# Optimization experiments

Measured on AMD Instinct MI355X. Metric: run time of the kernel, lower is better.

## Reference

```python
import jax, jax.numpy as jnp
import numpy as np

NZ = 128
N_GEN = 8
BATCH = 2048
SLOPE = 0.2


def _convt(x, w, b, stride, pad):
    # PyTorch ConvTranspose2d(weight [Cin,Cout,kH,kW], stride, padding p)
    # == conv with lhs_dilation=stride, padding=k-1-p, spatially-flipped
    # kernel with in/out channels swapped.
    k = jnp.flip(w, axis=(2, 3)).transpose(2, 3, 0, 1)  # [kH,kW,Cin,Cout]
    y = jax.lax.conv_general_dilated(
        x, k, window_strides=(1, 1), padding=[(pad, pad), (pad, pad)],
        lhs_dilation=(stride, stride),
        dimension_numbers=('NCHW', 'HWIO', 'NCHW'))
    return y + b[None, :, None, None]


def setup_inputs() -> dict:
    key = jax.random.key(0)
    ks = jax.random.split(key, 12)
    s = 0.05
    return {
        'z': jax.random.normal(ks[0], (BATCH, NZ), jnp.float32),
        'g_idx': jax.random.randint(ks[1], (BATCH,), 0, N_GEN),
        'W1': jax.random.normal(ks[2], (N_GEN, NZ, 256), jnp.float32) * s,
        'b1': jax.random.normal(ks[3], (N_GEN, 256), jnp.float32) * s,
        'W2': jax.random.normal(ks[4], (N_GEN, 256, 1568), jnp.float32) * s,
        'b2': jax.random.normal(ks[5], (N_GEN, 1568), jnp.float32) * s,
        'cw1': jax.random.normal(ks[6], (N_GEN, 32, 16, 4, 4), jnp.float32) * s,
        'cb1': jax.random.normal(ks[7], (N_GEN, 16), jnp.float32) * s,
        'cw2': jax.random.normal(ks[8], (N_GEN, 16, 8, 4, 4), jnp.float32) * s,
        'cb2': jax.random.normal(ks[9], (N_GEN, 8), jnp.float32) * s,
        'cw3': jax.random.normal(ks[10], (N_GEN, 8, 1, 3, 3), jnp.float32) * s,
        'cb3': jax.random.normal(ks[11], (N_GEN, 1), jnp.float32) * s,
    }


def _single_gen(params, z):
    W1, b1, W2, b2, cw1, cb1, cw2, cb2, cw3, cb3 = params
    lrelu = lambda x: jax.nn.leaky_relu(x, SLOPE)
    h = lrelu(z @ W1 + b1)                 # [B,256]
    h = lrelu(h @ W2 + b2)                 # [B,1568]
    h = h.reshape(-1, 32, 7, 7)
    h = lrelu(_convt(h, cw1, cb1, 2, 2))   # [B,16,14,14]
    h = lrelu(_convt(h, cw2, cb2, 2, 2))   # [B,8,28,28]
    return jnp.tanh(_convt(h, cw3, cb3, 1, 1))  # [B,1,28,28]


def reference(z, g_idx, W1, b1, W2, b2, cw1, cb1, cw2, cb2, cw3, cb3):
    params = (W1, b1, W2, b2, cw1, cb1, cw2, cb2, cw3, cb3)
    # Compute every generator on the full batch (faithful to the torch loop),
    # vmapped over the generator axis: images [G,B,1,28,28].
    images = jax.vmap(_single_gen, in_axes=((0,) * 10, None))(params, z)
    # Per-sample gather: keep generator g_idx[b] for each sample b.
    return images[g_idx, jnp.arange(z.shape[0])]
```

## Files before the change

### kernel.cpp

```cpp
#include <hip/hip_runtime.h>
#include <cstdint>
#include <cstddef>

#define BATCH 2048
#define NZ 128
#define NGEN 8
#define GRPS 32
#define MAXG 72
#define NCT 13
#define H2_ELEMS 1792
#define WS_H1_OFF 16384
#define WS_H2_OFF (16384 + MAXG * 8192 * 4)
#define WS_W2T_OFF (WS_H2_OFF + BATCH * H2_ELEMS * 2)
#define W2T_GSTRIDE (1568 * 256)
#define NB_W2T (NGEN * 49)
#define NB_PREP (NB_W2T + MAXG * 4)
#define WS_WPK1_OFF (WS_W2T_OFF + NGEN * W2T_GSTRIDE * 2)
#define WS_WPK2_OFF (WS_WPK1_OFF + NGEN * 4096 * 4)
#define WS_WPK3_OFF (WS_WPK2_OFF + NGEN * 1024 * 4)

typedef unsigned int u32;
typedef unsigned short u16;
typedef unsigned long long u64;
typedef _Float16 f16x8 __attribute__((ext_vector_type(8)));
typedef _Float16 f16x4 __attribute__((ext_vector_type(4)));
typedef _Float16 f16x2 __attribute__((ext_vector_type(2)));
typedef float f32x4 __attribute__((ext_vector_type(4)));

__device__ __forceinline__ float lrelu(float x) { return fmaxf(x, 0.2f * x); }
__device__ __forceinline__ u16 f16b(float f) {
    _Float16 h = (_Float16)f;
    return __builtin_bit_cast(u16, h);
}
__device__ __forceinline__ u32 pk2(float a, float b) {
    f16x2 v; v[0] = (_Float16)a; v[1] = (_Float16)b;
    return __builtin_bit_cast(u32, v);
}
__device__ __forceinline__ float dot2(u32 a, u32 b, float c) {
#if __has_builtin(__builtin_amdgcn_fdot2)
    return __builtin_amdgcn_fdot2(__builtin_bit_cast(f16x2, a),
                                  __builtin_bit_cast(f16x2, b), c, false);
#else
    float d;
    asm("v_dot2_f32_f16 %0, %1, %2, %3" : "=v"(d) : "v"(a), "v"(b), "v"(c));
    return d;
#endif
}
__device__ __forceinline__ float fast_tanh(float x) {
    x = fminf(fmaxf(x, -9.f), 9.f);
    const float e = __expf(2.f * x);
    return (e - 1.f) / (e + 1.f);
}

__global__ void bin_kernel(const int* __restrict__ g_idx, int* __restrict__ wsi) {
    __shared__ int wcnt[4][NGEN];
    __shared__ int wboff[4][NGEN];
    __shared__ int pbase[NGEN + 1];
    __shared__ u16 rank[BATCH];
    const int tid = threadIdx.x;
    const int w = tid >> 6, lane = tid & 63;
    if (tid < 4 * NGEN) wcnt[tid >> 3][tid & 7] = 0;
    __syncthreads();
    const u64 lt = ((u64)1 << lane) - 1;
    #pragma unroll
    for (int r = 0; r < 8; ++r) {
        const int b = r * 256 + tid;
        const int gg = g_idx[b];
        u64 m[NGEN];
        #pragma unroll
        for (int k = 0; k < NGEN; ++k) m[k] = __ballot(gg == k);
        rank[b] = (u16)((int)__popcll(m[gg] & lt) + wcnt[w][gg]);
        if (lane < NGEN) wcnt[w][lane] += (int)__popcll(m[lane]);
    }
    __syncthreads();
    if (tid == 0) {
        int acc = 0;
        for (int g = 0; g < NGEN; ++g) {
            pbase[g] = acc;
            const int tot = wcnt[0][g] + wcnt[1][g] + wcnt[2][g] + wcnt[3][g];
            acc += ((tot + GRPS - 1) / GRPS) * GRPS;
        }
        pbase[NGEN] = acc;
        wsi[0] = acc;
    }
    __syncthreads();
    if (tid < 32) {
        const int ww = tid >> 3, g = tid & 7;
        int off = pbase[g];
        for (int w2 = 0; w2 < ww; ++w2) off += wcnt[w2][g];
        wboff[ww][g] = off;
    }
    const int total = pbase[NGEN];
    for (int i = tid; i < total; i += 256) wsi[16 + i] = -1;
    __syncthreads();
    #pragma unroll
    for (int r = 0; r < 8; ++r) {
        const int b = r * 256 + tid;
        const int gg = g_idx[b];
        wsi[16 + wboff[w][gg] + (int)rank[b]] = b;
    }
}

__global__ __launch_bounds__(256) void prep_kernel(
    const float* __restrict__ z, const int* __restrict__ g_idx,
    const float* __restrict__ W1, const float* __restrict__ b1,
    const float* __restrict__ W2, const int* __restrict__ wsi,
    float* __restrict__ h1g, _Float16* __restrict__ W2T,
    const float* __restrict__ cw1, const float* __restrict__ cw2,
    const float* __restrict__ cw3,
    u32* __restrict__ wpk1, u32* __restrict__ wpk2, u32* __restrict__ wpk3)
{
    __shared__ _Float16 t[32][264];
    __shared__ float zst[NZ][12];
    __shared__ int sb[8];
    __shared__ int sG;

    const int tid = threadIdx.x;
    const int bx = blockIdx.x;

    if (bx >= NB_PREP) {
        const int g = bx - NB_PREP;
        const float* c1p = cw1 + g * 8192;
        u32* o1 = wpk1 + g * 4096;
        for (int i = tid; i < 4096; i += 256) {
            const int cip = i >> 8, a = (i >> 6) & 3, co = (i >> 2) & 15, c = i & 3;
            const float* s = c1p + cip * 512 + co * 16 + a * 4 + c;
            o1[i] = pk2(s[0], s[256]);
        }
        const float* c2p = cw2 + g * 2048;
        u32* o2 = wpk2 + g * 1024;
        for (int i = tid; i < 1024; i += 256) {
            const int cip = i >> 7, a = (i >> 5) & 3, co = (i >> 2) & 7, c = i & 3;
            const float* s = c2p + cip * 256 + co * 16 + a * 4 + c;
            o2[i] = pk2(s[0], s[128]);
        }
        if (tid < 36) {
            const int cip = tid / 9, r = tid % 9;
            const float* s = cw3 + g * 72 + cip * 18 + r;
            wpk3[g * 36 + tid] = pk2(s[0], s[9]);
        }
        return;
    }

    if (bx < NB_W2T) {
        const int g = bx / 49;
        const int n0 = (bx % 49) * 32;
        const float* src = W2 + (size_t)g * 256 * 1568;
        const int nl = tid & 31, kh = tid >> 5;
        #pragma unroll 8
        for (int p = 0; p < 32; ++p) {
            const int k = p * 8 + kh;
            t[nl][k] = (_Float16)src[(size_t)k * 1568 + n0 + nl];
        }
        __syncthreads();
        _Float16* dst = W2T + (size_t)g * W2T_GSTRIDE + (size_t)n0 * 256;
        const int n = tid >> 3, k0 = (tid & 7) * 32;
        #pragma unroll
        for (int j = 0; j < 4; ++j)
            *(uint4*)(dst + (size_t)n * 256 + k0 + 8 * j) = *(const uint4*)&t[n][k0 + 8 * j];
        return;
    }

    const int bx2 = bx - NB_W2T;
    const int grp = bx2 >> 2;
    const int s0 = (bx2 & 3) * 8;
    if (grp * GRPS >= wsi[0]) return;

    if (tid == 0) sG = g_idx[wsi[16 + grp * GRPS]];
    if (tid < 8) sb[tid] = wsi[16 + grp * GRPS + s0 + tid];
    __syncthreads();
    const float* W1g = W1 + sG * (NZ * 256);
    const float* b1g = b1 + sG * 256;

    {
        const int s = tid >> 5, f = tid & 31;
        float4 v = make_float4(0.f, 0.f, 0.f, 0.f);
        if (sb[s] >= 0) v = *(const float4*)(z + (size_t)sb[s] * NZ + 4 * f);
        zst[4 * f + 0][s] = v.x; zst[4 * f + 1][s] = v.y;
        zst[4 * f + 2][s] = v.z; zst[4 * f + 3][s] = v.w;
    }
    __syncthreads();

    const int c = tid;
    float acc[8];
    #pragma unroll
    for (int s = 0; s < 8; ++s) acc[s] = 0.f;
    const float* wp = W1g + c;
    #pragma unroll 4
    for (int k = 0; k < NZ; ++k) {
        const float w = wp[k * 256];
        float av[8];
        *(float4*)&av[0] = *(const float4*)&zst[k][0];
        *(float4*)&av[4] = *(const float4*)&zst[k][4];
        #pragma unroll
        for (int s = 0; s < 8; ++s) acc[s] += av[s] * w;
    }
    const float bv = b1g[c];
    float* hp = h1g + (size_t)grp * 8192 + (size_t)s0 * 256 + c;
    #pragma unroll
    for (int s = 0; s < 8; ++s) hp[s * 256] = lrelu(acc[s] + bv);
}

__global__ __launch_bounds__(256) void fc2_kernel(
    const int* __restrict__ g_idx,
    const _Float16* __restrict__ W2T, const float* __restrict__ b2,
    const int* __restrict__ wsi, const float* __restrict__ h1g,
    u16* __restrict__ h2g)
{
    __shared__ _Float16 afrag[2 * 8 * 64 * 8];
    __shared__ int sb[GRPS];
    __shared__ int sG;

    const int tid = threadIdx.x;
    const int grp = blockIdx.x / NCT;
    const int tile = blockIdx.x % NCT;
    if (grp * GRPS >= wsi[0]) return;

    if (tid == 0) sG = g_idx[wsi[16 + grp * GRPS]];
    if (tid < GRPS) sb[tid] = wsi[16 + grp * GRPS + tid];
    __syncthreads();
    const _Float16* W2Tg = W2T + (size_t)sG * W2T_GSTRIDE;
    const float* b2g = b2 + sG * 1568;

    {
        const float4* h1p4 = (const float4*)(h1g + (size_t)grp * 8192);
        #pragma unroll
        for (int i = 0; i < 8; ++i) {
            const int u = tid + 256 * i;
            const int j4 = u & 1;
            const int ln = (u >> 1) & 63;
            const int kq = (u >> 7) & 7;
            const int mt = (u >> 10) & 1;
            const int s = mt * 16 + (ln & 15);
            const float4 v = h1p4[s * 64 + kq * 8 + ((ln >> 4) << 1) + j4];
            f16x4 hi;
            hi[0] = (_Float16)v.x; hi[1] = (_Float16)v.y;
            hi[2] = (_Float16)v.z; hi[3] = (_Float16)v.w;
            const int bh = ((mt * 8 + kq) * 64 + ln) * 8 + 4 * j4;
            *(f16x4*)&afrag[bh] = hi;
        }
    }
    __syncthreads();

    const int wave = tid >> 6;
    const int lane = tid & 63;
    const int q = lane >> 4;
    const int nl = lane & 15;
    const int nb0 = tile * 128 + 2 * wave * 16;
    if (nb0 >= 1568) return;

    #pragma unroll
    for (int nt = 0; nt < 2; ++nt) {
        const int nb = nb0 + nt * 16;
        if (nb >= 1568) break;
        const int n = nb + nl;
        const _Float16* bp = W2Tg + (size_t)n * 256 + q * 8;
        f32x4 accA = {0.f, 0.f, 0.f, 0.f}, accB = accA;
        #pragma unroll
        for (int kq = 0; kq < 8; ++kq) {
            const f16x8 b = *(const f16x8*)(bp + kq * 32);
            const f16x8 a0 = *(const f16x8*)&afrag[((0 * 8 + kq) * 64 + lane) * 8];
            const f16x8 a1 = *(const f16x8*)&afrag[((1 * 8 + kq) * 64 + lane) * 8];
            accA = __builtin_amdgcn_mfma_f32_16x16x32_f16(a0, b, accA, 0, 0, 0);
            accB = __builtin_amdgcn_mfma_f32_16x16x32_f16(a1, b, accB, 0, 0, 0);
        }
        const float bias = b2g[n];
        const int ci = n / 49, rm = n % 49;
        const int off = ci * 56 + (rm / 7) * 8 + (rm % 7);
        #pragma unroll
        for (int mt = 0; mt < 2; ++mt) {
            const f32x4 a = (mt == 0) ? accA : accB;
            #pragma unroll
            for (int reg = 0; reg < 4; ++reg) {
                const int s = mt * 16 + q * 4 + reg;
                const int bb = sb[s];
                if (bb >= 0)
                    h2g[(size_t)bb * H2_ELEMS + off] = f16b(lrelu(a[reg] + bias));
            }
        }
    }
}

template <int H>
__device__ __forceinline__ void conv2p_half(
    const u32 (*c1s)[14][20], u16* dst,
    const u32* __restrict__ w2g, const float bv, const int co, const int y)
{
    float acc[14];
    #pragma unroll
    for (int xx = 0; xx < 14; ++xx) acc[xx] = bv;
    const int a0 = (y + 1) & 1;
    for (int aa = 0; aa < 2; ++aa) {
        const int a = a0 + 2 * aa;
        const int iy = (y + 1 - a) >> 1;
        if ((unsigned)iy < 14u) {
            #pragma unroll 2
            for (int cip = 0; cip < 8; ++cip) {
                u32 rr[10];
                if (H == 0) {
                    *(uint4*)&rr[0] = *(const uint4*)&c1s[cip][iy][0];
                    *(uint4*)&rr[4] = *(const uint4*)&c1s[cip][iy][4];
                } else {
                    *(uint4*)&rr[0] = *(const uint4*)&c1s[cip][iy][4];
                    *(uint4*)&rr[4] = *(const uint4*)&c1s[cip][iy][8];
                    *(uint2*)&rr[8] = *(const uint2*)&c1s[cip][iy][12];
                }
                const uint4 wq = *(const uint4*)(w2g + ((cip * 4 + a) * 8 + co) * 4);
                const u32 wv[4] = {wq.x, wq.y, wq.z, wq.w};
                #pragma unroll
                for (int xx = 0; xx < 14; ++xx) {
                    const int x = 14 * H + xx;
                    const int c0v = (x + 1) & 1;
                    const int ix0 = (x + 1 - c0v) >> 1;
                    const int li = ix0 - 4 * H;
                    if (ix0 < 14) acc[xx] = dot2(rr[li],     wv[c0v],     acc[xx]);
                    if (ix0 >= 1) acc[xx] = dot2(rr[li - 1], wv[c0v + 2], acc[xx]);
                }
            }
        }
    }
    #pragma unroll
    for (int xx = 0; xx < 14; ++xx) dst[2 * (14 * H + xx)] = f16b(lrelu(acc[xx]));
}

__global__ __launch_bounds__(256, 7) void conv_kernel(
    const int* __restrict__ g_idx,
    const u32* __restrict__ wpk1, const float* __restrict__ cb1,
    const u32* __restrict__ wpk2, const float* __restrict__ cb2,
    const u32* __restrict__ wpk3, const float* __restrict__ cb3,
    const u16* __restrict__ h2g, float* __restrict__ out)
{
    __shared__ __align__(16) char smem[8960 + 12992];
    u32 (*c1s)[14][20] = (u32 (*)[14][20])smem;
    u32 (*h2s)[7][8]   = (u32 (*)[7][8])(smem + 8960);
    u32 (*c2s)[28][29] = (u32 (*)[28][29])(smem + 8960);
    __shared__ u32 w3s[36];

    const int tid = threadIdx.x;
    const int b = blockIdx.x;
    const int g = g_idx[b];
    const u32* w1g = wpk1 + g * 4096;
    const u32* w2g = wpk2 + g * 1024;
    const float* cb1g = cb1 + g * 16;
    const float* cb2g = cb2 + g * 8;
    const float  cb3v = cb3[g];

    if (tid < 224) {
        const uint4 qv = ((const uint4*)(h2g + (size_t)b * H2_ELEMS))[tid];
        const int ci = tid / 7, yq = tid % 7;
        u16* dst = (u16*)&h2s[ci >> 1][yq][0] + (ci & 1);
        const u32 w[4] = {qv.x, qv.y, qv.z, qv.w};
        #pragma unroll
        for (int j = 0; j < 4; ++j) {
            dst[4 * j]     = (u16)(w[j] & 0xffffu);
            dst[4 * j + 2] = (u16)(w[j] >> 16);
        }
    }
    if (tid < 36) w3s[tid] = wpk3[g * 36 + tid];
    __syncthreads();

    if (tid < 224) {
        const int co = tid / 14, y = tid % 14;
        const float bv = cb1g[co];
        float acc[14];
        #pragma unroll
        for (int x = 0; x < 14; ++x) acc[x] = bv;
        const int a0 = (y + 1) & 1;
        for (int aa = 0; aa < 2; ++aa) {
            const int a = a0 + 2 * aa;
            const int iy = (y + 1 - a) >> 1;
            if ((unsigned)iy < 7u) {
                #pragma unroll 2
                for (int cip = 0; cip < 16; ++cip) {
                    u32 rr[8];
                    *(uint4*)&rr[0] = *(const uint4*)&h2s[cip][iy][0];
                    *(uint4*)&rr[4] = *(const uint4*)&h2s[cip][iy][4];
                    const uint4 wq = *(const uint4*)(w1g + ((cip * 4 + a) * 16 + co) * 4);
                    const u32 wv[4] = {wq.x, wq.y, wq.z, wq.w};
                    #pragma unroll
                    for (int x = 0; x < 14; ++x) {
                        const int c0v = (x + 1) & 1;
                        const int ix0 = (x + 1 - c0v) >> 1;
                        if (ix0 < 7)  acc[x] = dot2(rr[ix0],     wv[c0v],     acc[x]);
                        if (ix0 >= 1) acc[x] = dot2(rr[ix0 - 1], wv[c0v + 2], acc[x]);
                    }
                }
            }
        }
        u16* dst = (u16*)&c1s[co >> 1][y][0] + (co & 1);
        #pragma unroll
        for (int x = 0; x < 14; ++x) dst[2 * x] = f16b(lrelu(acc[x]));
    }
    __syncthreads();

    if (tid < 224) {
        const int co = tid / 28, y = tid % 28;
        const float bv = cb2g[co];
        u16* dst = (u16*)&c2s[co >> 1][y][0] + (co & 1);
        conv2p_half<0>(c1s, dst, w2g, bv, co, y);
        conv2p_half<1>(c1s, dst, w2g, bv, co, y);
    }
    __syncthreads();

    if (tid < 196) {
        const int y = tid / 7, qq = tid % 7;
        const int xb = qq * 4;
        float acc[4] = {cb3v, cb3v, cb3v, cb3v};
        #pragma unroll 2
        for (int cip = 0; cip < 4; ++cip) {
            u32 wp[9];
            #pragma unroll
            for (int j = 0; j < 9; ++j) wp[j] = w3s[cip * 9 + j];
            #pragma unroll
            for (int a = 0; a < 3; ++a) {
                const int iy = y + 1 - a;
                if ((unsigned)iy < 28u) {
                    u32 rr[6];
                    #pragma unroll
                    for (int j = 0; j < 6; ++j) {
                        const int ix = xb - 1 + j;
                        rr[j] = ((unsigned)ix < 28u) ? c2s[cip][iy][ix] : 0u;
                    }
                    #pragma unroll
                    for (int xx = 0; xx < 4; ++xx)
                        #pragma unroll
                        for (int c = 0; c < 3; ++c)
                            acc[xx] = dot2(rr[xx + 2 - c], wp[a * 3 + c], acc[xx]);
                }
            }
        }
        float* op = out + (size_t)b * 784 + y * 28 + xb;
        #pragma unroll
        for (int xx = 0; xx < 4; ++xx) op[xx] = fast_tanh(acc[xx]);
    }
}

extern "C" void kernel_launch(void* const* d_in, const int* in_sizes, int n_in,
                              void* d_out, int out_size, void* d_ws, size_t ws_size,
                              hipStream_t stream) {
    const float* z   = (const float*)d_in[0];
    const int*   gi  = (const int*)d_in[1];
    const float* W1  = (const float*)d_in[2];
    const float* b1  = (const float*)d_in[3];
    const float* W2  = (const float*)d_in[4];
    const float* b2  = (const float*)d_in[5];
    const float* cw1 = (const float*)d_in[6];
    const float* cb1 = (const float*)d_in[7];
    const float* cw2 = (const float*)d_in[8];
    const float* cb2 = (const float*)d_in[9];
    const float* cw3 = (const float*)d_in[10];
    const float* cb3 = (const float*)d_in[11];
    int*      wsi = (int*)d_ws;
    float*    h1g = (float*)((char*)d_ws + WS_H1_OFF);
    u16*      h2g = (u16*)((char*)d_ws + WS_H2_OFF);
    _Float16* w2t = (_Float16*)((char*)d_ws + WS_W2T_OFF);
    u32*      wpk1 = (u32*)((char*)d_ws + WS_WPK1_OFF);
    u32*      wpk2 = (u32*)((char*)d_ws + WS_WPK2_OFF);
    u32*      wpk3 = (u32*)((char*)d_ws + WS_WPK3_OFF);

    bin_kernel<<<1, 256, 0, stream>>>(gi, wsi);
    prep_kernel<<<NB_PREP + NGEN, 256, 0, stream>>>(z, gi, W1, b1, W2, wsi, h1g, w2t,
                                                    cw1, cw2, cw3, wpk1, wpk2, wpk3);
    fc2_kernel<<<MAXG * NCT, 256, 0, stream>>>(gi, w2t, b2, wsi, h1g, h2g);
    conv_kernel<<<BATCH, 256, 0, stream>>>(gi, wpk1, cb1, wpk2, cb2, wpk3, cb3,
                                           h2g, (float*)d_out);
}
```

Before: 166.4 us.

## Stage fc2 outputs in shared memory and write h2 rows with vector stores

The fc2 epilogue now writes its results into a shared-memory staging tile, which replaces the scattered 2-byte global stores per sample. Each sample's contiguous h2 span is then copied to global memory as uint4 stores, with scalar stores only at the unaligned edges. The W2 transpose store loop is reindexed so consecutive threads write consecutive 16-byte chunks. The conv kernel pads its c2s row stride from 29 to 33 and lowers the launch-bounds occupancy hint from 7 to 6, which adds shared memory per block and may reduce resident blocks.

Result: faster. 161.2 us (-3.2%).

```diff
diff --git a/kernel.cpp b/kernel.cpp
--- a/kernel.cpp
+++ b/kernel.cpp
@@ -18,6 +18,7 @@
 #define WS_WPK1_OFF (WS_W2T_OFF + NGEN * W2T_GSTRIDE * 2)
 #define WS_WPK2_OFF (WS_WPK1_OFF + NGEN * 4096 * 4)
 #define WS_WPK3_OFF (WS_WPK2_OFF + NGEN * 1024 * 4)
+#define PS 168
 
 typedef unsigned int u32;
 typedef unsigned short u16;
@@ -50,6 +51,10 @@
     x = fminf(fmaxf(x, -9.f), 9.f);
     const float e = __expf(2.f * x);
     return (e - 1.f) / (e + 1.f);
+}
+__device__ __forceinline__ int h2off(int n) {
+    const int ci = n / 49, rm = n % 49;
+    return ci * 56 + (rm / 7) * 8 + (rm % 7);
 }
 
 __global__ void bin_kernel(const int* __restrict__ g_idx, int* __restrict__ wsi) {
@@ -154,10 +159,12 @@
         }
         __syncthreads();
         _Float16* dst = W2T + (size_t)g * W2T_GSTRIDE + (size_t)n0 * 256;
-        const int n = tid >> 3, k0 = (tid & 7) * 32;
-        #pragma unroll
-        for (int j = 0; j < 4; ++j)
-            *(uint4*)(dst + (size_t)n * 256 + k0 + 8 * j) = *(const uint4*)&t[n][k0 + 8 * j];
+        #pragma unroll
+        for (int ii = 0; ii < 4; ++ii) {
+            const int i = tid + 256 * ii;
+            const int n = i >> 5, kc = i & 31;
+            *(uint4*)(dst + (size_t)n * 256 + kc * 8) = *(const uint4*)&t[n][kc * 8];
+        }
         return;
     }
 
@@ -207,7 +214,8 @@
     const int* __restrict__ wsi, const float* __restrict__ h1g,
     u16* __restrict__ h2g)
 {
-    __shared__ _Float16 afrag[2 * 8 * 64 * 8];
+    __shared__ __align__(16) char afsm[16384];
+    _Float16* afrag = (_Float16*)afsm;
     __shared__ int sb[GRPS];
     __shared__ int sG;
 
@@ -247,36 +255,76 @@
     const int q = lane >> 4;
     const int nl = lane & 15;
     const int nb0 = tile * 128 + 2 * wave * 16;
-    if (nb0 >= 1568) return;
-
-    #pragma unroll
-    for (int nt = 0; nt < 2; ++nt) {
-        const int nb = nb0 + nt * 16;
-        if (nb >= 1568) break;
-        const int n = nb + nl;
-        const _Float16* bp = W2Tg + (size_t)n * 256 + q * 8;
-        f32x4 accA = {0.f, 0.f, 0.f, 0.f}, accB = accA;
+    const int nb1 = nb0 + 16;
+    const bool act0 = nb0 < 1568, act1 = nb1 < 1568;
+
+    f32x4 accA0 = {0.f, 0.f, 0.f, 0.f}, accB0 = accA0;
+    f32x4 accA1 = accA0, accB1 = accA0;
+    if (act0) {
+        const _Float16* bp = W2Tg + (size_t)(nb0 + nl) * 256 + q * 8;
         #pragma unroll
         for (int kq = 0; kq < 8; ++kq) {
             const f16x8 b = *(const f16x8*)(bp + kq * 32);
             const f16x8 a0 = *(const f16x8*)&afrag[((0 * 8 + kq) * 64 + lane) * 8];
             const f16x8 a1 = *(const f16x8*)&afrag[((1 * 8 + kq) * 64 + lane) * 8];
-            accA = __builtin_amdgcn_mfma_f32_16x16x32_f16(a0, b, accA, 0, 0, 0);
-            accB = __builtin_amdgcn_mfma_f32_16x16x32_f16(a1, b, accB, 0, 0, 0);
-        }
+            accA0 = __builtin_amdgcn_mfma_f32_16x16x32_f16(a0, b, accA0, 0, 0, 0);
+            accB0 = __builtin_amdgcn_mfma_f32_16x16x32_f16(a1, b, accB0, 0, 0, 0);
+        }
+    }
+    if (act1) {
+        const _Float16* bp = W2Tg + (size_t)(nb1 + nl) * 256 + q * 8;
+        #pragma unroll
+        for (int kq = 0; kq < 8; ++kq) {
+            const f16x8 b = *(const f16x8*)(bp + kq * 32);
+            const f16x8 a0 = *(const f16x8*)&afrag[((0 * 8 + kq) * 64 + lane) * 8];
+            const f16x8 a1 = *(const f16x8*)&afrag[((1 * 8 + kq) * 64 + lane) * 8];
+            accA1 = __builtin_amdgcn_mfma_f32_16x16x32_f16(a0, b, accA1, 0, 0, 0);
+            accB1 = __builtin_amdgcn_mfma_f32_16x16x32_f16(a1, b, accB1, 0, 0, 0);
+        }
+    }
+    __syncthreads();
+
+    u16* pst = (u16*)afsm;
+    const int nstart = tile * 128;
+    const int nend = (nstart + 128 < 1568) ? nstart + 128 : 1568;
+    const int offLo = h2off(nstart), offHi = h2off(nend - 1);
+    const int lo8 = offLo & ~7;
+
+    if (act0) {
+        const int n = nb0 + nl;
         const float bias = b2g[n];
-        const int ci = n / 49, rm = n % 49;
-        const int off = ci * 56 + (rm / 7) * 8 + (rm % 7);
-        #pragma unroll
-        for (int mt = 0; mt < 2; ++mt) {
-            const f32x4 a = (mt == 0) ? accA : accB;
-            #pragma unroll
-            for (int reg = 0; reg < 4; ++reg) {
-                const int s = mt * 16 + q * 4 + reg;
-                const int bb = sb[s];
-                if (bb >= 0)
-                    h2g[(size_t)bb * H2_ELEMS + off] = f16b(lrelu(a[reg] + bias));
-            }
+        u16* pp = pst + (h2off(n) - lo8);
+        #pragma unroll
+        for (int reg = 0; reg < 4; ++reg) {
+            pp[(q * 4 + reg) * PS]        = f16b(lrelu(accA0[reg] + bias));
+            pp[(16 + q * 4 + reg) * PS]   = f16b(lrelu(accB0[reg] + bias));
+        }
+    }
+    if (act1) {
+        const int n = nb1 + nl;
+        const float bias = b2g[n];
+        u16* pp = pst + (h2off(n) - lo8);
+        #pragma unroll
+        for (int reg = 0; reg < 4; ++reg) {
+            pp[(q * 4 + reg) * PS]        = f16b(lrelu(accA1[reg] + bias));
+            pp[(16 + q * 4 + reg) * PS]   = f16b(lrelu(accB1[reg] + bias));
+        }
+    }
+    __syncthreads();
+
+    {
+        const int s = tid >> 3, p = tid & 7;
+        const int bb = sb[s];
+        if (bb >= 0) {
+            u16* row = h2g + (size_t)bb * H2_ELEMS;
+            const u16* ps = pst + s * PS - lo8;
+            const int c0 = (offLo + 7) & ~7;
+            const int c1 = (offHi + 1) & ~7;
+            for (int o = offLo + p; o < c0 && o <= offHi; o += 8) row[o] = ps[o];
+            const int t0 = (c1 > offLo) ? c1 : offLo;
+            for (int o = t0 + p; o <= offHi; o += 8) row[o] = ps[o];
+            for (int c = c0 + p * 8; c + 8 <= c1; c += 64)
+                *(uint4*)(row + c) = *(const uint4*)(ps + c);
         }
     }
 }
@@ -323,17 +371,17 @@
     for (int xx = 0; xx < 14; ++xx) dst[2 * (14 * H + xx)] = f16b(lrelu(acc[xx]));
 }
 
-__global__ __launch_bounds__(256, 7) void conv_kernel(
+__global__ __launch_bounds__(256, 6) void conv_kernel(
     const int* __restrict__ g_idx,
     const u32* __restrict__ wpk1, const float* __restrict__ cb1,
     const u32* __restrict__ wpk2, const float* __restrict__ cb2,
     const u32* __restrict__ wpk3, const float* __restrict__ cb3,
     const u16* __restrict__ h2g, float* __restrict__ out)
 {
-    __shared__ __align__(16) char smem[8960 + 12992];
+    __shared__ __align__(16) char smem[8960 + 14784];
     u32 (*c1s)[14][20] = (u32 (*)[14][20])smem;
     u32 (*h2s)[7][8]   = (u32 (*)[7][8])(smem + 8960);
-    u32 (*c2s)[28][29] = (u32 (*)[28][29])(smem + 8960);
+    u32 (*c2s)[28][33] = (u32 (*)[28][33])(smem + 8960);
     __shared__ u32 w3s[36];
 
     const int tid = threadIdx.x;
```
